# Kernel tuning notes

Measured on AMD Instinct MI355X. Metric: run time of the kernel, lower is better.

Reference implementation:

```python
import jax, jax.numpy as jnp
import numpy as np

NEIGHBOR_N = 3


def setup_inputs() -> dict:
    key = jax.random.key(0)
    ks = jax.random.split(key, 4)
    B, D = 8192, 512
    H = D // 2
    sess_emb = jax.random.normal(ks[0], (B, D), dtype=jnp.float32)
    pool_emb = jax.random.normal(ks[1], (1024, D), dtype=jnp.float32)
    # torch Linear default init ~ U(-1/sqrt(fan_in), 1/sqrt(fan_in)); scaled normals ok as baseline
    W1 = jax.random.normal(ks[2], (D, H), dtype=jnp.float32) / np.sqrt(D)
    b1 = jnp.zeros((H,), dtype=jnp.float32)
    W2 = jax.random.normal(ks[3], (H, D), dtype=jnp.float32) / np.sqrt(H)
    b2 = jnp.zeros((D,), dtype=jnp.float32)
    return {"sess_emb": sess_emb, "pool_emb": pool_emb, "W1": W1, "b1": b1, "W2": W2, "b2": b2}


def reference(sess_emb, pool_emb, W1, b1, W2, b2):
    # scoring MLP (dropout = identity in eval mode)
    h = jax.nn.relu(sess_emb @ W1 + b1)          # (B, D/2)
    sess_proj = h @ W2 + b2                       # (B, D)
    # self-similarity and top-k neighbors
    sim_matrix = sess_proj @ sess_proj.T          # (B, B)
    cos_topk, topk_indice = jax.lax.top_k(sim_matrix, NEIGHBOR_N)  # (B, K)
    sess_topk = sess_emb[topk_indice]             # (B, K, D) gather
    cos_topk = jax.nn.softmax(cos_topk, axis=-1)  # (B, K)
    neighbor_sess = jnp.einsum('bk,bkd->bd', cos_topk, sess_topk)  # (B, D)
    return (sess_topk, neighbor_sess, cos_topk)
```

## Files before the change

### kernel.cpp

```cpp
#include <hip/hip_runtime.h>
#include <hip/hip_bf16.h>
#include <math.h>

#define NB 8192
#define DD 512
#define HH 256
#define TB 128
#define BK 32
#define BK2 64
#define KT2 (DD / BK2)
#define NSLOT 64
#define ROWKEYS (NSLOT * 3)
#define NCAND 8
#define NTRI 2080

typedef unsigned short ushortT;
typedef __attribute__((ext_vector_type(8))) short bf16x8;
typedef __attribute__((ext_vector_type(4))) float f32x4;

#define AS1(p) ((const __attribute__((address_space(1))) void*)(p))
#define AS3(p) ((__attribute__((address_space(3))) void*)(p))

__device__ __forceinline__ ushortT bf16rne(float f) {
    unsigned u = __float_as_uint(f);
    unsigned r = u + 0x7FFFu + ((u >> 16) & 1u);
    return (ushortT)(r >> 16);
}
__device__ __forceinline__ float bf16tof(ushortT h) {
    return __uint_as_float(((unsigned)h) << 16);
}

__global__ __launch_bounds__(256)
void prep_kernel(const float* __restrict__ sess, const float* __restrict__ W1,
                 const float* __restrict__ W2,
                 ushortT* __restrict__ sess_hi, ushortT* __restrict__ sess_lo,
                 ushortT* __restrict__ w1t_hi, ushortT* __restrict__ w1t_lo,
                 ushortT* __restrict__ w2t_hi, ushortT* __restrict__ w2t_lo) {
    const int b = blockIdx.x, t = threadIdx.x;
    if (b < 2048) {
        size_t i = (size_t)b * 2048 + t * 8;
        float4 f0 = *(const float4*)&sess[i];
        float4 f1 = *(const float4*)&sess[i + 4];
        float f[8] = {f0.x, f0.y, f0.z, f0.w, f1.x, f1.y, f1.z, f1.w};
        unsigned hp[4], lp[4];
#pragma unroll
        for (int j = 0; j < 4; ++j) {
            ushortT h0 = bf16rne(f[2 * j]), h1 = bf16rne(f[2 * j + 1]);
            ushortT l0 = bf16rne(f[2 * j] - bf16tof(h0));
            ushortT l1 = bf16rne(f[2 * j + 1] - bf16tof(h1));
            hp[j] = (unsigned)h0 | ((unsigned)h1 << 16);
            lp[j] = (unsigned)l0 | ((unsigned)l1 << 16);
        }
        *(uint4*)&sess_hi[i] = *(uint4*)hp;
        *(uint4*)&sess_lo[i] = *(uint4*)lp;
    } else if (b < 2112) {
        int o = (b - 2048) * 2048 + t * 8;
        int k = o >> 8, c = o & 255;
        float4 f0 = *(const float4*)&W1[(size_t)k * 256 + c];
        float4 f1 = *(const float4*)&W1[(size_t)k * 256 + c + 4];
        float f[8] = {f0.x, f0.y, f0.z, f0.w, f1.x, f1.y, f1.z, f1.w};
#pragma unroll
        for (int j = 0; j < 8; ++j) {
            ushortT h = bf16rne(f[j]);
            w1t_hi[(size_t)(c + j) * 512 + k] = h;
            w1t_lo[(size_t)(c + j) * 512 + k] = bf16rne(f[j] - bf16tof(h));
        }
    } else {
        int o = (b - 2112) * 2048 + t * 8;
        int k = o >> 9, c = o & 511;
        float4 f0 = *(const float4*)&W2[(size_t)k * 512 + c];
        float4 f1 = *(const float4*)&W2[(size_t)k * 512 + c + 4];
        float f[8] = {f0.x, f0.y, f0.z, f0.w, f1.x, f1.y, f1.z, f1.w};
#pragma unroll
        for (int j = 0; j < 8; ++j) {
            ushortT h = bf16rne(f[j]);
            w2t_hi[(size_t)(c + j) * 256 + k] = h;
            w2t_lo[(size_t)(c + j) * 256 + k] = bf16rne(f[j] - bf16tof(h));
        }
    }
}

template <int KDIM, int NOUT, int EPI, int TM>
__global__ __launch_bounds__(256)
void mlp_gemm(const ushortT* __restrict__ Ahi, const ushortT* __restrict__ Alo,
              const ushortT* __restrict__ Bhi, const ushortT* __restrict__ Blo,
              const float* __restrict__ bias,
              ushortT* __restrict__ Ohi, ushortT* __restrict__ Olo,
              float* __restrict__ Of, ushortT* __restrict__ Ob) {
    constexpr int AC = TM / 16;
    constexpr int CHUNKS = 2 * AC + 32;
    constexpr int QN = CHUNKS / 4;
    constexpr int BUFS = CHUNKS * 512;
    constexpr int MI = TM / 32;
    __shared__ short gsmem[2 * BUFS];
    const int KTILES = KDIM / BK;
    const int t = threadIdx.x;
    const int w = t >> 6, l = t & 63;
    const int wr = w >> 1, wc = w & 1;
    const int tx = l & 15, tg = l >> 4;
    const int rb = blockIdx.x * TM;
    const int cb = blockIdx.y * 256;

    const int rin = l >> 2;
    const int tgs = (l & 3) ^ ((rin >> 1) & 3);
    const int loff = tx * BK + ((tg ^ ((tx >> 1) & 3)) << 3);

    f32x4 acc[MI][8];
#pragma unroll
    for (int i = 0; i < MI; ++i)
#pragma unroll
        for (int j = 0; j < 8; ++j) acc[i][j] = (f32x4){0.f, 0.f, 0.f, 0.f};

#define GSTAGE(buf, k0v)                                                                     \
    {                                                                                        \
        _Pragma("unroll")                                                                    \
        for (int q = 0; q < QN; ++q) {                                                       \
            int c = w * QN + q;                                                              \
            const ushortT* src; int row; int lofs;                                           \
            if (c < AC)            { src = Ahi; row = rb + c * 16 + rin;             lofs = c * 512; }                  \
            else if (c < 2 * AC)   { src = Alo; row = rb + (c - AC) * 16 + rin;      lofs = c * 512; }                  \
            else if (c < 2*AC+16)  { src = Bhi; row = cb + (c - 2*AC) * 16 + rin;    lofs = c * 512; }                  \
            else                   { src = Blo; row = cb + (c - 2*AC - 16) * 16 + rin; lofs = c * 512; }                \
            const ushortT* g = src + (size_t)row * KDIM + (k0v) + tgs * 8;                   \
            __builtin_amdgcn_global_load_lds(AS1(g), AS3(gsmem + (buf) * BUFS + lofs + l * 8), 16, 0, 0); \
        }                                                                                    \
    }

#define GCOMPUTE(kt)                                                                         \
    {                                                                                        \
        const short* Bu = gsmem + ((kt) & 1) * BUFS;                                         \
        bf16x8 ah[MI], al[MI], bh[8], bl[8];                                                 \
        _Pragma("unroll")                                                                    \
        for (int mi = 0; mi < MI; ++mi) {                                                    \
            ah[mi] = *(const bf16x8*)&Bu[(wr * MI + mi) * 512 + loff];                       \
            al[mi] = *(const bf16x8*)&Bu[AC * 512 + (wr * MI + mi) * 512 + loff];            \
        }                                                                                    \
        _Pragma("unroll")                                                                    \
        for (int nj = 0; nj < 8; ++nj) {                                                     \
            bh[nj] = *(const bf16x8*)&Bu[2 * AC * 512 + (wc * 8 + nj) * 512 + loff];         \
            bl[nj] = *(const bf16x8*)&Bu[(2 * AC + 16) * 512 + (wc * 8 + nj) * 512 + loff];  \
        }                                                                                    \
        asm volatile("s_waitcnt lgkmcnt(0)" ::: "memory");                                   \
        __builtin_amdgcn_sched_barrier(0);                                                   \
        __builtin_amdgcn_s_barrier();                                                        \
        __builtin_amdgcn_sched_barrier(0);                                                   \
        _Pragma("unroll")                                                                    \
        for (int mi = 0; mi < MI; ++mi)                                                      \
            _Pragma("unroll")                                                                \
            for (int nj = 0; nj < 8; ++nj) {                                                 \
                acc[mi][nj] = __builtin_amdgcn_mfma_f32_16x16x32_bf16(ah[mi], bh[nj], acc[mi][nj], 0, 0, 0); \
                acc[mi][nj] = __builtin_amdgcn_mfma_f32_16x16x32_bf16(ah[mi], bl[nj], acc[mi][nj], 0, 0, 0); \
                acc[mi][nj] = __builtin_amdgcn_mfma_f32_16x16x32_bf16(al[mi], bh[nj], acc[mi][nj], 0, 0, 0); \
            }                                                                                \
    }

    GSTAGE(0, 0);
    for (int kt = 0; kt < KTILES - 1; ++kt) {
        GSTAGE((kt + 1) & 1, (kt + 1) * BK);
        if constexpr (TM == 64) { asm volatile("s_waitcnt vmcnt(10)" ::: "memory"); }
        else                    { asm volatile("s_waitcnt vmcnt(9)" ::: "memory"); }
        __builtin_amdgcn_sched_barrier(0);
        __builtin_amdgcn_s_barrier();
        __builtin_amdgcn_sched_barrier(0);
        GCOMPUTE(kt);
    }
    asm volatile("s_waitcnt vmcnt(0)" ::: "memory");
    __builtin_amdgcn_sched_barrier(0);
    __builtin_amdgcn_s_barrier();
    __builtin_amdgcn_sched_barrier(0);
    GCOMPUTE(KTILES - 1);
#undef GSTAGE
#undef GCOMPUTE

#pragma unroll
    for (int mi = 0; mi < MI; ++mi) {
#pragma unroll
        for (int nj = 0; nj < 8; ++nj) {
            int col = cb + wc * 128 + nj * 16 + tx;
            float bv = bias[col];
#pragma unroll
            for (int rr = 0; rr < 4; ++rr) {
                int row = rb + wr * (TM / 2) + mi * 16 + tg * 4 + rr;
                float v = acc[mi][nj][rr] + bv;
                if (EPI == 0) {
                    v = fmaxf(v, 0.f);
                    ushortT h = bf16rne(v);
                    Ohi[(size_t)row * NOUT + col] = h;
                    Olo[(size_t)row * NOUT + col] = bf16rne(v - bf16tof(h));
                } else {
                    Of[(size_t)row * NOUT + col] = v;
                    Ob[(size_t)row * NOUT + col] = bf16rne(v);
                }
            }
        }
    }
}

__device__ __forceinline__ void ins3k(unsigned key, unsigned& k0, unsigned& k1, unsigned& k2) {
    bool g0 = key > k0, g1 = key > k1, g2 = key > k2;
    k2 = g1 ? k1 : (g2 ? key : k2);
    k1 = g0 ? k0 : (g1 ? key : k1);
    k0 = g0 ? key : k0;
}
__device__ __forceinline__ void merge3k(unsigned& a0, unsigned& a1, unsigned& a2,
                                        unsigned b0, unsigned b1, unsigned b2) {
    unsigned m0 = a0 > b0 ? a0 : b0;
    bool c0 = a0 > b0;
    unsigned ca1 = c0 ? a1 : b1;
    unsigned cb0 = c0 ? b0 : a0;
    unsigned ca2 = c0 ? a2 : b2;
    unsigned cb1 = c0 ? b1 : a1;
    bool c1 = ca1 > cb0;
    unsigned m1 = c1 ? ca1 : cb0;
    unsigned x = c1 ? ca2 : ca1;
    unsigned y = c1 ? cb0 : cb1;
    unsigned m2 = x > y ? x : y;
    a0 = m0; a1 = m1; a2 = m2;
}
__device__ __forceinline__ unsigned packkey(float f, unsigned idx) {
    unsigned u = __float_as_uint(f);
    unsigned tt = (unsigned)((int)u >> 31) | 0x80000000u;
    return ((u ^ tt) & 0xFFFFE000u) | (8191u - idx);
}

__global__ __launch_bounds__(256)
void sim_mfma_kernel(const short* __restrict__ projb, unsigned* __restrict__ pkeys) {
    const int b = blockIdx.x;
    const int L = (b & 7) * 260 + (b >> 3);
    int rem = L, si = 0, sj = 0;
    for (;;) {
        int n = (si == sj) ? 36 : 64;
        if (rem < n) break;
        rem -= n;
        if (si == sj) { si = 0; ++sj; } else { ++si; }
    }
    int ci, cj;
    if (si == sj) {
        cj = 0;
        while (rem >= cj + 1) { rem -= cj + 1; ++cj; }
        ci = rem;
    } else { ci = rem & 7; cj = rem >> 3; }
    const int ib = si * 8 + ci;
    const int jbk = sj * 8 + cj;
    const bool do_tr = (ib < jbk);

    __shared__ short smem[2 * TB * BK2 * 2];
    short* As = smem;
    short* Bs = smem + 2 * TB * BK2;
    unsigned* evu = (unsigned*)smem;
    unsigned* evt = (unsigned*)smem + 3200;

    const int t = threadIdx.x;
    const int w = t >> 6, l = t & 63;
    const int wr = w >> 1, wc = w & 1;
    const int tx = l & 15, tg = l >> 4;
    const int rb = ib * TB;
    const int jb = jbk * TB;

    const int sl8 = (((l & 7) ^ (l >> 3)) << 3);
    const int sw0 = (((0 + tg) ^ (tx & 7)) << 3);
    const int sw1 = (((4 + tg) ^ (tx & 7)) << 3);

    f32x4 acc[4][4];
#pragma unroll
    for (int i = 0; i < 4; ++i)
#pragma unroll
        for (int j = 0; j < 4; ++j) acc[i][j] = (f32x4){0.f, 0.f, 0.f, 0.f};

#define STAGE(buf, k0)                                                                      \
    {                                                                                       \
        _Pragma("unroll")                                                                   \
        for (int q = 0; q < 4; ++q) {                                                       \
            int c = w * 4 + q;                                                              \
            const short* ga = projb + (size_t)(rb + c * 8 + (l >> 3)) * DD + (k0) + sl8;    \
            __builtin_amdgcn_global_load_lds(AS1(ga), AS3(As + (buf) * 8192 + c * 512 + l * 8), 16, 0, 0); \
            const short* gb = projb + (size_t)(jb + c * 8 + (l >> 3)) * DD + (k0) + sl8;    \
            __builtin_amdgcn_global_load_lds(AS1(gb), AS3(Bs + (buf) * 8192 + c * 512 + l * 8), 16, 0, 0); \
        }                                                                                   \
    }

#define COMPUTE(kt)                                                                          \
    {                                                                                        \
        const short* Ab = As + ((kt) & 1) * 8192;                                            \
        const short* Bb = Bs + ((kt) & 1) * 8192;                                            \
        bf16x8 af0[4], af1[4], bf0[4], bf1[4];                                               \
        _Pragma("unroll")                                                                    \
        for (int mi = 0; mi < 4; ++mi) {                                                     \
            int row = wr * 64 + mi * 16 + tx;                                                \
            af0[mi] = *(const bf16x8*)&Ab[row * 64 + sw0];                                   \
            af1[mi] = *(const bf16x8*)&Ab[row * 64 + sw1];                                   \
        }                                                                                    \
        _Pragma("unroll")                                                                    \
        for (int nj = 0; nj < 4; ++nj) {                                                     \
            int row = wc * 64 + nj * 16 + tx;                                                \
            bf0[nj] = *(const bf16x8*)&Bb[row * 64 + sw0];                                   \
            bf1[nj] = *(const bf16x8*)&Bb[row * 64 + sw1];                                   \
        }                                                                                    \
        asm volatile("s_waitcnt lgkmcnt(0)" ::: "memory");                                   \
        __builtin_amdgcn_sched_barrier(0);                                                   \
        __builtin_amdgcn_s_barrier();                                                        \
        __builtin_amdgcn_sched_barrier(0);                                                   \
        _Pragma("unroll")                                                                    \
        for (int mi = 0; mi < 4; ++mi)                                                       \
            _Pragma("unroll")                                                                \
            for (int nj = 0; nj < 4; ++nj)                                                   \
                acc[mi][nj] = __builtin_amdgcn_mfma_f32_16x16x32_bf16(af0[mi], bf0[nj], acc[mi][nj], 0, 0, 0); \
        _Pragma("unroll")                                                                    \
        for (int mi = 0; mi < 4; ++mi)                                                       \
            _Pragma("unroll")                                                                \
            for (int nj = 0; nj < 4; ++nj)                                                   \
                acc[mi][nj] = __builtin_amdgcn_mfma_f32_16x16x32_bf16(af1[mi], bf1[nj], acc[mi][nj], 0, 0, 0); \
    }

    STAGE(0, 0);
    for (int kt = 0; kt < KT2 - 1; ++kt) {
        STAGE((kt + 1) & 1, (kt + 1) * BK2);
        asm volatile("s_waitcnt vmcnt(8)" ::: "memory");
        __builtin_amdgcn_sched_barrier(0);
        __builtin_amdgcn_s_barrier();
        __builtin_amdgcn_sched_barrier(0);
        COMPUTE(kt);
    }
    asm volatile("s_waitcnt vmcnt(0)" ::: "memory");
    __builtin_amdgcn_sched_barrier(0);
    __builtin_amdgcn_s_barrier();
    __builtin_amdgcn_sched_barrier(0);
    COMPUTE(KT2 - 1);
#undef STAGE
#undef COMPUTE

    __syncthreads();

    unsigned cinv[4];
#pragma unroll
    for (int nj = 0; nj < 4; ++nj)
        cinv[nj] = 8191u - (unsigned)(jb + wc * 64 + nj * 16 + tx);
#pragma unroll
    for (int mi = 0; mi < 4; ++mi) {
#pragma unroll
        for (int rr = 0; rr < 4; ++rr) {
            unsigned k0 = 0, k1 = 0, k2 = 0;
#pragma unroll
            for (int nj = 0; nj < 4; ++nj) {
                unsigned u = __float_as_uint(acc[mi][nj][rr]);
                unsigned tt = (unsigned)((int)u >> 31) | 0x80000000u;
                ins3k(((u ^ tt) & 0xFFFFE000u) | cinv[nj], k0, k1, k2);
            }
#pragma unroll
            for (int s = 1; s <= 2; s <<= 1) {
                unsigned b0 = (unsigned)__shfl_xor((int)k0, s, 64);
                unsigned b1 = (unsigned)__shfl_xor((int)k1, s, 64);
                unsigned b2 = (unsigned)__shfl_xor((int)k2, s, 64);
                merge3k(k0, k1, k2, b0, b1, b2);
            }
            if ((tx & 3) == 0) {
                int lrow = wr * 64 + mi * 16 + tg * 4 + rr;
                unsigned* e = &evu[lrow * 25 + (wc * 4 + (tx >> 2)) * 3];
                e[0] = k0; e[1] = k1; e[2] = k2;
            }
        }
    }

    if (do_tr) {
#pragma unroll
        for (int nj = 0; nj < 4; ++nj) {
            unsigned k0 = 0, k1 = 0, k2 = 0;
#pragma unroll
            for (int mi = 0; mi < 4; ++mi) {
#pragma unroll
                for (int rr = 0; rr < 4; ++rr) {
                    unsigned idx = (unsigned)(rb + wr * 64 + mi * 16 + tg * 4 + rr);
                    ins3k(packkey(acc[mi][nj][rr], idx), k0, k1, k2);
                }
            }
#pragma unroll
            for (int s = 16; s <= 32; s <<= 1) {
                unsigned b0 = (unsigned)__shfl_xor((int)k0, s, 64);
                unsigned b1 = (unsigned)__shfl_xor((int)k1, s, 64);
                unsigned b2 = (unsigned)__shfl_xor((int)k2, s, 64);
                merge3k(k0, k1, k2, b0, b1, b2);
            }
            if (tg == 0) {
                int col = wc * 64 + nj * 16 + tx;
                unsigned* e = &evt[col * 6 + wr * 3];
                e[0] = k0; e[1] = k1; e[2] = k2;
            }
        }
    }
    __syncthreads();

    if (t < TB) {
        unsigned k0 = 0, k1 = 0, k2 = 0;
        const unsigned* e = &evu[t * 25];
#pragma unroll
        for (int s = 0; s < 24; ++s) ins3k(e[s], k0, k1, k2);
        unsigned* pk = pkeys + (size_t)(rb + t) * ROWKEYS + jbk * 3;
        pk[0] = k0; pk[1] = k1; pk[2] = k2;
    }
    if (do_tr && t < TB) {
        unsigned k0 = 0, k1 = 0, k2 = 0;
        const unsigned* e = &evt[t * 6];
#pragma unroll
        for (int s = 0; s < 6; ++s) ins3k(e[s], k0, k1, k2);
        unsigned* pk = pkeys + (size_t)(jb + t) * ROWKEYS + ib * 3;
        pk[0] = k0; pk[1] = k1; pk[2] = k2;
    }
}

__global__ __launch_bounds__(256)
void rerank_out_kernel(const float* __restrict__ proj, const unsigned* __restrict__ pkeys,
                       const float* __restrict__ sess, float* __restrict__ out,
                       float* __restrict__ cos_out) {
    int r = blockIdx.x * 4 + (threadIdx.x >> 6);
    int t = threadIdx.x & 63;
    const unsigned* pk = pkeys + (size_t)r * ROWKEYS;
    unsigned a0 = pk[3 * t], a1 = pk[3 * t + 1], a2 = pk[3 * t + 2];
    {
        unsigned m01 = a0 > a1 ? a0 : a1, n01 = a0 > a1 ? a1 : a0;
        unsigned m2 = n01 > a2 ? n01 : a2, n2 = n01 > a2 ? a2 : n01;
        a0 = m01 > m2 ? m01 : m2;
        a1 = m01 > m2 ? m2 : m01;
        a2 = n2;
    }
    unsigned ck[NCAND];
#pragma unroll
    for (int i = 0; i < NCAND; ++i) {
        unsigned m = a0;
#pragma unroll
        for (int s = 1; s < 64; s <<= 1) {
            unsigned o = (unsigned)__shfl_xor((int)m, s, 64);
            m = m > o ? m : o;
        }
        ck[i] = m;
        if (a0 == m) { a0 = a1; a1 = a2; a2 = 0; }
    }
    int cj[NCAND];
#pragma unroll
    for (int i = 0; i < NCAND; ++i) cj[i] = 8191 - (int)(ck[i] & 0x1FFFu);

    const float* pr = proj + (size_t)r * DD;
    float myp[8];
#pragma unroll
    for (int k = 0; k < 8; ++k) myp[k] = pr[t * 8 + k];
    double part[NCAND];
#pragma unroll
    for (int i = 0; i < NCAND; ++i) {
        const float* pc = proj + (size_t)cj[i] * DD;
        double s = 0.0;
#pragma unroll
        for (int k = 0; k < 8; ++k) s += (double)myp[k] * (double)pc[t * 8 + k];
        part[i] = s;
    }
#pragma unroll
    for (int i = 0; i < NCAND; ++i) {
#pragma unroll
        for (int s = 1; s < 64; s <<= 1) part[i] += __shfl_xor(part[i], s, 64);
    }
    double bv0 = -1e300, bv1 = -1e300, bv2 = -1e300;
    int bj0 = 0x7fffffff, bj1 = 0x7fffffff, bj2 = 0x7fffffff;
#pragma unroll
    for (int i = 0; i < NCAND; ++i) {
        double v = part[i]; int j = cj[i];
        bool g2 = (v > bv2) || (v == bv2 && j < bj2);
        bool g1 = (v > bv1) || (v == bv1 && j < bj1);
        bool g0 = (v > bv0) || (v == bv0 && j < bj0);
        if (g2) {
            if (g1) {
                if (g0) { bv2 = bv1; bj2 = bj1; bv1 = bv0; bj1 = bj0; bv0 = v; bj0 = j; }
                else    { bv2 = bv1; bj2 = bj1; bv1 = v; bj1 = j; }
            } else      { bv2 = v; bj2 = j; }
        }
    }
    double e1 = exp(bv1 - bv0), e2 = exp(bv2 - bv0);
    double inv = 1.0 / (1.0 + e1 + e2);
    float w0 = (float)inv, w1 = (float)(e1 * inv), w2 = (float)(e2 * inv);
    if (t == 0) {
        cos_out[r * 3 + 0] = w0; cos_out[r * 3 + 1] = w1; cos_out[r * 3 + 2] = w2;
    }
    const float4* s0 = (const float4*)(sess + (size_t)bj0 * DD);
    const float4* s1 = (const float4*)(sess + (size_t)bj1 * DD);
    const float4* s2 = (const float4*)(sess + (size_t)bj2 * DD);
    float4* o = (float4*)(out + (size_t)r * 3 * DD);
    float4* nb = (float4*)(out + (size_t)NB * 3 * DD + (size_t)r * DD);
#pragma unroll
    for (int e = 0; e < 2; ++e) {
        int q = t + e * 64;
        float4 x0 = s0[q], x1 = s1[q], x2 = s2[q];
        o[q] = x0; o[128 + q] = x1; o[256 + q] = x2;
        float4 v;
        v.x = fmaf(w0, x0.x, fmaf(w1, x1.x, w2 * x2.x));
        v.y = fmaf(w0, x0.y, fmaf(w1, x1.y, w2 * x2.y));
        v.z = fmaf(w0, x0.z, fmaf(w1, x1.z, w2 * x2.z));
        v.w = fmaf(w0, x0.w, fmaf(w1, x1.w, w2 * x2.w));
        nb[q] = v;
    }
}

extern "C" void kernel_launch(void* const* d_in, const int* in_sizes, int n_in,
                              void* d_out, int out_size, void* d_ws, size_t ws_size,
                              hipStream_t stream) {
    const float* sess = (const float*)d_in[0];
    const float* W1 = (const float*)d_in[2];
    const float* b1 = (const float*)d_in[3];
    const float* W2 = (const float*)d_in[4];
    const float* b2 = (const float*)d_in[5];
    float* out = (float*)d_out;

    const size_t MBc = 1u << 20;
    char* W = (char*)d_ws;
    float*   proj    = (float*)W;
    ushortT* sess_hi = (ushortT*)W;
    ushortT* sess_lo = sess_hi + (size_t)NB * DD;
    ushortT* projb   = (ushortT*)(W + 16 * MBc);
    ushortT* h_hi    = (ushortT*)(W + 24 * MBc);
    ushortT* h_lo    = (ushortT*)(W + 28 * MBc);
    ushortT* w1t_hi  = (ushortT*)(W + 32 * MBc);
    ushortT* w1t_lo  = w1t_hi + 256 * 512;
    ushortT* w2t_hi  = w1t_lo + 256 * 512;
    ushortT* w2t_lo  = w2t_hi + 512 * 256;
    unsigned* pkeys  = (unsigned*)(W + 24 * MBc);

    float* cos_out = out + (size_t)NB * 3 * DD + (size_t)NB * DD;

    hipLaunchKernelGGL(prep_kernel, dim3(2176), dim3(256), 0, stream,
                       sess, W1, W2, sess_hi, sess_lo, w1t_hi, w1t_lo, w2t_hi, w2t_lo);
    hipLaunchKernelGGL((mlp_gemm<512, 256, 0, 32>), dim3(NB / 32, 1), dim3(256), 0, stream,
                       sess_hi, sess_lo, w1t_hi, w1t_lo, b1, h_hi, h_lo, (float*)nullptr, (ushortT*)nullptr);
    hipLaunchKernelGGL((mlp_gemm<256, 512, 1, 64>), dim3(NB / 64, 2), dim3(256), 0, stream,
                       h_hi, h_lo, w2t_hi, w2t_lo, b2, (ushortT*)nullptr, (ushortT*)nullptr, proj, projb);
    hipLaunchKernelGGL(sim_mfma_kernel, dim3(NTRI), dim3(256), 0, stream,
                       (const short*)projb, pkeys);
    hipLaunchKernelGGL(rerank_out_kernel, dim3(NB / 4), dim3(256), 0, stream,
                       proj, pkeys, sess, out, cos_out);
}
```

Baseline: 145.3 us.

## Make sim kernel persistent over four tiles with cross-tile prefetch

The similarity kernel now launches 520 blocks, each handling four consecutive upper-triangle tiles. The first k-slab of the next tile is prefetched during the last compute step of the current one, hiding load latency at tile boundaries. Epilogue buffers move to dedicated LDS so they no longer alias the staging buffers, and top-3 selection uses a sorting network plus merges instead of sequential inserts. This adds LDS use, which may lower occupancy, and an extra barrier per k-step.

Result: slower. 179.3 us (+23.4%).

```diff
diff --git a/kernel.cpp b/kernel.cpp
--- a/kernel.cpp
+++ b/kernel.cpp
@@ -12,7 +12,7 @@
 #define NSLOT 64
 #define ROWKEYS (NSLOT * 3)
 #define NCAND 8
-#define NTRI 2080
+#define NBLK 520
 
 typedef unsigned short ushortT;
 typedef __attribute__((ext_vector_type(8))) short bf16x8;
@@ -196,6 +196,8 @@
     }
 }
 
+__device__ __forceinline__ unsigned umaxu(unsigned a, unsigned b) { return a > b ? a : b; }
+__device__ __forceinline__ unsigned uminu(unsigned a, unsigned b) { return a < b ? a : b; }
 __device__ __forceinline__ void ins3k(unsigned key, unsigned& k0, unsigned& k1, unsigned& k2) {
     bool g0 = key > k0, g1 = key > k1, g2 = key > k2;
     k2 = g1 ? k1 : (g2 ? key : k2);
@@ -217,16 +219,25 @@
     unsigned m2 = x > y ? x : y;
     a0 = m0; a1 = m1; a2 = m2;
 }
+__device__ __forceinline__ void top3of4(unsigned a, unsigned b, unsigned c, unsigned d,
+                                        unsigned& k0, unsigned& k1, unsigned& k2) {
+    unsigned s1 = umaxu(a, b), t1 = uminu(a, b);
+    unsigned s2 = umaxu(c, d), t2 = uminu(c, d);
+    bool cw = s1 > s2;
+    unsigned c2 = cw ? s2 : s1;
+    unsigned tw = cw ? t1 : t2;
+    unsigned tl = cw ? t2 : t1;
+    k0 = cw ? s1 : s2;
+    k1 = umaxu(c2, tw);
+    k2 = umaxu(uminu(c2, tw), tl);
+}
 __device__ __forceinline__ unsigned packkey(float f, unsigned idx) {
     unsigned u = __float_as_uint(f);
     unsigned tt = (unsigned)((int)u >> 31) | 0x80000000u;
     return ((u ^ tt) & 0xFFFFE000u) | (8191u - idx);
 }
 
-__global__ __launch_bounds__(256)
-void sim_mfma_kernel(const short* __restrict__ projb, unsigned* __restrict__ pkeys) {
-    const int b = blockIdx.x;
-    const int L = (b & 7) * 260 + (b >> 3);
+__device__ __forceinline__ void decodeL(int L, int& ib, int& jbk) {
     int rem = L, si = 0, sj = 0;
     for (;;) {
         int n = (si == sj) ? 36 : 64;
@@ -240,171 +251,183 @@
         while (rem >= cj + 1) { rem -= cj + 1; ++cj; }
         ci = rem;
     } else { ci = rem & 7; cj = rem >> 3; }
-    const int ib = si * 8 + ci;
-    const int jbk = sj * 8 + cj;
-    const bool do_tr = (ib < jbk);
-
+    ib = si * 8 + ci;
+    jbk = sj * 8 + cj;
+}
+
+__global__ __launch_bounds__(256)
+void sim_mfma_kernel(const short* __restrict__ projb, unsigned* __restrict__ pkeys) {
     __shared__ short smem[2 * TB * BK2 * 2];
+    __shared__ unsigned evu[TB * 25];
+    __shared__ unsigned evt[TB * 6];
     short* As = smem;
     short* Bs = smem + 2 * TB * BK2;
-    unsigned* evu = (unsigned*)smem;
-    unsigned* evt = (unsigned*)smem + 3200;
+
+    const int b = blockIdx.x;
+    const int base = ((b & 7) * 65 + (b >> 3)) * 4;
 
     const int t = threadIdx.x;
     const int w = t >> 6, l = t & 63;
     const int wr = w >> 1, wc = w & 1;
     const int tx = l & 15, tg = l >> 4;
-    const int rb = ib * TB;
-    const int jb = jbk * TB;
 
     const int sl8 = (((l & 7) ^ (l >> 3)) << 3);
     const int sw0 = (((0 + tg) ^ (tx & 7)) << 3);
     const int sw1 = (((4 + tg) ^ (tx & 7)) << 3);
 
-    f32x4 acc[4][4];
-#pragma unroll
-    for (int i = 0; i < 4; ++i)
-#pragma unroll
-        for (int j = 0; j < 4; ++j) acc[i][j] = (f32x4){0.f, 0.f, 0.f, 0.f};
-
-#define STAGE(buf, k0)                                                                      \
+#define STAGE(buf, k0, RB, JB)                                                              \
     {                                                                                       \
         _Pragma("unroll")                                                                   \
-        for (int q = 0; q < 4; ++q) {                                                       \
-            int c = w * 4 + q;                                                              \
-            const short* ga = projb + (size_t)(rb + c * 8 + (l >> 3)) * DD + (k0) + sl8;    \
+        for (int qq = 0; qq < 4; ++qq) {                                                    \
+            int c = w * 4 + qq;                                                             \
+            const short* ga = projb + (size_t)((RB) + c * 8 + (l >> 3)) * DD + (k0) + sl8;  \
             __builtin_amdgcn_global_load_lds(AS1(ga), AS3(As + (buf) * 8192 + c * 512 + l * 8), 16, 0, 0); \
-            const short* gb = projb + (size_t)(jb + c * 8 + (l >> 3)) * DD + (k0) + sl8;    \
+            const short* gb = projb + (size_t)((JB) + c * 8 + (l >> 3)) * DD + (k0) + sl8;  \
             __builtin_amdgcn_global_load_lds(AS1(gb), AS3(Bs + (buf) * 8192 + c * 512 + l * 8), 16, 0, 0); \
         }                                                                                   \
     }
 
-#define COMPUTE(kt)                                                                          \
-    {                                                                                        \
-        const short* Ab = As + ((kt) & 1) * 8192;                                            \
-        const short* Bb = Bs + ((kt) & 1) * 8192;                                            \
-        bf16x8 af0[4], af1[4], bf0[4], bf1[4];                                               \
-        _Pragma("unroll")                                                                    \
-        for (int mi = 0; mi < 4; ++mi) {                                                     \
-            int row = wr * 64 + mi * 16 + tx;                                                \
-            af0[mi] = *(const bf16x8*)&Ab[row * 64 + sw0];                                   \
-            af1[mi] = *(const bf16x8*)&Ab[row * 64 + sw1];                                   \
-        }                                                                                    \
-        _Pragma("unroll")                                                                    \
-        for (int nj = 0; nj < 4; ++nj) {                                                     \
-            int row = wc * 64 + nj * 16 + tx;                                                \
-            bf0[nj] = *(const bf16x8*)&Bb[row * 64 + sw0];                                   \
-            bf1[nj] = *(const bf16x8*)&Bb[row * 64 + sw1];                                   \
-        }                                                                                    \
-        asm volatile("s_waitcnt lgkmcnt(0)" ::: "memory");                                   \
-        __builtin_amdgcn_sched_barrier(0);                                                   \
-        __builtin_amdgcn_s_barrier();                                                        \
-        __builtin_amdgcn_sched_barrier(0);                                                   \
-        _Pragma("unroll")                                                                    \
-        for (int mi = 0; mi < 4; ++mi)                                                       \
-            _Pragma("unroll")                                                                \
-            for (int nj = 0; nj < 4; ++nj)                                                   \
-                acc[mi][nj] = __builtin_amdgcn_mfma_f32_16x16x32_bf16(af0[mi], bf0[nj], acc[mi][nj], 0, 0, 0); \
-        _Pragma("unroll")                                                                    \
-        for (int mi = 0; mi < 4; ++mi)                                                       \
-            _Pragma("unroll")                                                                \
-            for (int nj = 0; nj < 4; ++nj)                                                   \
-                acc[mi][nj] = __builtin_amdgcn_mfma_f32_16x16x32_bf16(af1[mi], bf1[nj], acc[mi][nj], 0, 0, 0); \
-    }
-
-    STAGE(0, 0);
-    for (int kt = 0; kt < KT2 - 1; ++kt) {
-        STAGE((kt + 1) & 1, (kt + 1) * BK2);
-        asm volatile("s_waitcnt vmcnt(8)" ::: "memory");
-        __builtin_amdgcn_sched_barrier(0);
-        __builtin_amdgcn_s_barrier();
-        __builtin_amdgcn_sched_barrier(0);
-        COMPUTE(kt);
-    }
-    asm volatile("s_waitcnt vmcnt(0)" ::: "memory");
-    __builtin_amdgcn_sched_barrier(0);
-    __builtin_amdgcn_s_barrier();
-    __builtin_amdgcn_sched_barrier(0);
-    COMPUTE(KT2 - 1);
+    int ib, jbk;
+    decodeL(base, ib, jbk);
+    int rb = ib * TB, jb = jbk * TB;
+    STAGE(0, 0, rb, jb);
+
+    for (int q = 0; q < 4; ++q) {
+        const bool do_tr = (ib < jbk);
+        int nib = 0, njbk = 0;
+        if (q < 3) decodeL(base + q + 1, nib, njbk);
+
+        f32x4 acc[4][4];
+#pragma unroll
+        for (int i = 0; i < 4; ++i)
+#pragma unroll
+            for (int j = 0; j < 4; ++j) acc[i][j] = (f32x4){0.f, 0.f, 0.f, 0.f};
+
+        for (int kt = 0; kt < KT2; ++kt) {
+            if (kt + 1 < KT2) { STAGE((kt + 1) & 1, (kt + 1) * BK2, rb, jb); }
+            else if (q < 3)   { STAGE(0, 0, nib * TB, njbk * TB); }
+            if (kt + 1 < KT2 || q < 3) { asm volatile("s_waitcnt vmcnt(8)" ::: "memory"); }
+            else                       { asm volatile("s_waitcnt vmcnt(0)" ::: "memory"); }
+            __builtin_amdgcn_sched_barrier(0);
+            __builtin_amdgcn_s_barrier();
+            __builtin_amdgcn_sched_barrier(0);
+            {
+                const short* Ab = As + (kt & 1) * 8192;
+                const short* Bb = Bs + (kt & 1) * 8192;
+                bf16x8 af0[4], af1[4], bf0[4], bf1[4];
+#pragma unroll
+                for (int mi = 0; mi < 4; ++mi) {
+                    int row = wr * 64 + mi * 16 + tx;
+                    af0[mi] = *(const bf16x8*)&Ab[row * 64 + sw0];
+                    af1[mi] = *(const bf16x8*)&Ab[row * 64 + sw1];
+                }
+#pragma unroll
+                for (int nj = 0; nj < 4; ++nj) {
+                    int row = wc * 64 + nj * 16 + tx;
+                    bf0[nj] = *(const bf16x8*)&Bb[row * 64 + sw0];
+                    bf1[nj] = *(const bf16x8*)&Bb[row * 64 + sw1];
+                }
+#pragma unroll
+                for (int mi = 0; mi < 4; ++mi)
+#pragma unroll
+                    for (int nj = 0; nj < 4; ++nj)
+                        acc[mi][nj] = __builtin_amdgcn_mfma_f32_16x16x32_bf16(af0[mi], bf0[nj], acc[mi][nj], 0, 0, 0);
+#pragma unroll
+                for (int mi = 0; mi < 4; ++mi)
+#pragma unroll
+                    for (int nj = 0; nj < 4; ++nj)
+                        acc[mi][nj] = __builtin_amdgcn_mfma_f32_16x16x32_bf16(af1[mi], bf1[nj], acc[mi][nj], 0, 0, 0);
+            }
+            __builtin_amdgcn_sched_barrier(0);
+            __builtin_amdgcn_s_barrier();
+            __builtin_amdgcn_sched_barrier(0);
+        }
+
+        unsigned cinv[4];
+#pragma unroll
+        for (int nj = 0; nj < 4; ++nj)
+            cinv[nj] = 8191u - (unsigned)(jb + wc * 64 + nj * 16 + tx);
+#pragma unroll
+        for (int mi = 0; mi < 4; ++mi) {
+#pragma unroll
+            for (int rr = 0; rr < 4; ++rr) {
+                unsigned kk[4];
+#pragma unroll
+                for (int nj = 0; nj < 4; ++nj) {
+                    unsigned u = __float_as_uint(acc[mi][nj][rr]);
+                    unsigned tt = (unsigned)((int)u >> 31) | 0x80000000u;
+                    kk[nj] = ((u ^ tt) & 0xFFFFE000u) | cinv[nj];
+                }
+                unsigned k0, k1, k2;
+                top3of4(kk[0], kk[1], kk[2], kk[3], k0, k1, k2);
+#pragma unroll
+                for (int s = 1; s <= 2; s <<= 1) {
+                    unsigned b0 = (unsigned)__shfl_xor((int)k0, s, 64);
+                    unsigned b1 = (unsigned)__shfl_xor((int)k1, s, 64);
+                    unsigned b2 = (unsigned)__shfl_xor((int)k2, s, 64);
+                    merge3k(k0, k1, k2, b0, b1, b2);
+                }
+                if ((tx & 3) == 0) {
+                    int lrow = wr * 64 + mi * 16 + tg * 4 + rr;
+                    unsigned* e = &evu[lrow * 25 + (wc * 4 + (tx >> 2)) * 3];
+                    e[0] = k0; e[1] = k1; e[2] = k2;
+                }
+            }
+        }
+
+        if (do_tr) {
+#pragma unroll
+            for (int nj = 0; nj < 4; ++nj) {
+                unsigned v[16];
+#pragma unroll
+                for (int mi = 0; mi < 4; ++mi)
+#pragma unroll
+                    for (int rr = 0; rr < 4; ++rr) {
+                        unsigned idx = (unsigned)(rb + wr * 64 + mi * 16 + tg * 4 + rr);
+                        v[mi * 4 + rr] = packkey(acc[mi][nj][rr], idx);
+                    }
+                unsigned x0, x1, x2, y0, y1, y2, z0, z1, z2;
+                top3of4(v[0], v[1], v[2], v[3], x0, x1, x2);
+                top3of4(v[4], v[5], v[6], v[7], y0, y1, y2);
+                merge3k(x0, x1, x2, y0, y1, y2);
+                top3of4(v[8], v[9], v[10], v[11], y0, y1, y2);
+                top3of4(v[12], v[13], v[14], v[15], z0, z1, z2);
+                merge3k(y0, y1, y2, z0, z1, z2);
+                merge3k(x0, x1, x2, y0, y1, y2);
+#pragma unroll
+                for (int s = 16; s <= 32; s <<= 1) {
+                    unsigned b0 = (unsigned)__shfl_xor((int)x0, s, 64);
+                    unsigned b1 = (unsigned)__shfl_xor((int)x1, s, 64);
+                    unsigned b2 = (unsigned)__shfl_xor((int)x2, s, 64);
+                    merge3k(x0, x1, x2, b0, b1, b2);
+                }
+                if (tg == 0) {
+                    int col = wc * 64 + nj * 16 + tx;
+                    unsigned* e = &evt[col * 6 + wr * 3];
+                    e[0] = x0; e[1] = x1; e[2] = x2;
+                }
+            }
+        }
+        __syncthreads();
+
+        if (t < TB) {
+            const unsigned* e = &evu[t * 25];
+            unsigned k0 = e[0], k1 = e[1], k2 = e[2];
+#pragma unroll
+            for (int s = 1; s < 8; ++s) merge3k(k0, k1, k2, e[s * 3], e[s * 3 + 1], e[s * 3 + 2]);
+            unsigned* pk = pkeys + (size_t)(rb + t) * ROWKEYS + jbk * 3;
+            pk[0] = k0; pk[1] = k1; pk[2] = k2;
+        }
+        if (do_tr && t < TB) {
+            const unsigned* e = &evt[t * 6];
+            unsigned k0 = e[0], k1 = e[1], k2 = e[2];
+            merge3k(k0, k1, k2, e[3], e[4], e[5]);
+            unsigned* pk = pkeys + (size_t)(jb + t) * ROWKEYS + ib * 3;
+            pk[0] = k0; pk[1] = k1; pk[2] = k2;
+        }
+        ib = nib; jbk = njbk; rb = ib * TB; jb = jbk * TB;
+    }
 #undef STAGE
-#undef COMPUTE
-
-    __syncthreads();
-
-    unsigned cinv[4];
-#pragma unroll
-    for (int nj = 0; nj < 4; ++nj)
-        cinv[nj] = 8191u - (unsigned)(jb + wc * 64 + nj * 16 + tx);
-#pragma unroll
-    for (int mi = 0; mi < 4; ++mi) {
-#pragma unroll
-        for (int rr = 0; rr < 4; ++rr) {
-            unsigned k0 = 0, k1 = 0, k2 = 0;
-#pragma unroll
-            for (int nj = 0; nj < 4; ++nj) {
-                unsigned u = __float_as_uint(acc[mi][nj][rr]);
-                unsigned tt = (unsigned)((int)u >> 31) | 0x80000000u;
-                ins3k(((u ^ tt) & 0xFFFFE000u) | cinv[nj], k0, k1, k2);
-            }
-#pragma unroll
-            for (int s = 1; s <= 2; s <<= 1) {
-                unsigned b0 = (unsigned)__shfl_xor((int)k0, s, 64);
-                unsigned b1 = (unsigned)__shfl_xor((int)k1, s, 64);
-                unsigned b2 = (unsigned)__shfl_xor((int)k2, s, 64);
-                merge3k(k0, k1, k2, b0, b1, b2);
-            }
-            if ((tx & 3) == 0) {
-                int lrow = wr * 64 + mi * 16 + tg * 4 + rr;
-                unsigned* e = &evu[lrow * 25 + (wc * 4 + (tx >> 2)) * 3];
-                e[0] = k0; e[1] = k1; e[2] = k2;
-            }
-        }
-    }
-
-    if (do_tr) {
-#pragma unroll
-        for (int nj = 0; nj < 4; ++nj) {
-            unsigned k0 = 0, k1 = 0, k2 = 0;
-#pragma unroll
-            for (int mi = 0; mi < 4; ++mi) {
-#pragma unroll
-                for (int rr = 0; rr < 4; ++rr) {
-                    unsigned idx = (unsigned)(rb + wr * 64 + mi * 16 + tg * 4 + rr);
-                    ins3k(packkey(acc[mi][nj][rr], idx), k0, k1, k2);
-                }
-            }
-#pragma unroll
-            for (int s = 16; s <= 32; s <<= 1) {
-                unsigned b0 = (unsigned)__shfl_xor((int)k0, s, 64);
-                unsigned b1 = (unsigned)__shfl_xor((int)k1, s, 64);
-                unsigned b2 = (unsigned)__shfl_xor((int)k2, s, 64);
-                merge3k(k0, k1, k2, b0, b1, b2);
-            }
-            if (tg == 0) {
-                int col = wc * 64 + nj * 16 + tx;
-                unsigned* e = &evt[col * 6 + wr * 3];
-                e[0] = k0; e[1] = k1; e[2] = k2;
-            }
-        }
-    }
-    __syncthreads();
-
-    if (t < TB) {
-        unsigned k0 = 0, k1 = 0, k2 = 0;
-        const unsigned* e = &evu[t * 25];
-#pragma unroll
-        for (int s = 0; s < 24; ++s) ins3k(e[s], k0, k1, k2);
-        unsigned* pk = pkeys + (size_t)(rb + t) * ROWKEYS + jbk * 3;
-        pk[0] = k0; pk[1] = k1; pk[2] = k2;
-    }
-    if (do_tr && t < TB) {
-        unsigned k0 = 0, k1 = 0, k2 = 0;
-        const unsigned* e = &evt[t * 6];
-#pragma unroll
-        for (int s = 0; s < 6; ++s) ins3k(e[s], k0, k1, k2);
-        unsigned* pk = pkeys + (size_t)(jb + t) * ROWKEYS + ib * 3;
-        pk[0] = k0; pk[1] = k1; pk[2] = k2;
-    }
 }
 
 __global__ __launch_bounds__(256)
@@ -528,7 +551,7 @@
                        sess_hi, sess_lo, w1t_hi, w1t_lo, b1, h_hi, h_lo, (float*)nullptr, (ushortT*)nullptr);
     hipLaunchKernelGGL((mlp_gemm<256, 512, 1, 64>), dim3(NB / 64, 2), dim3(256), 0, stream,
                        h_hi, h_lo, w2t_hi, w2t_lo, b2, (ushortT*)nullptr, (ushortT*)nullptr, proj, projb);
-    hipLaunchKernelGGL(sim_mfma_kernel, dim3(NTRI), dim3(256), 0, stream,
+    hipLaunchKernelGGL(sim_mfma_kernel, dim3(NBLK), dim3(256), 0, stream,
                        (const short*)projb, pkeys);
     hipLaunchKernelGGL(rerank_out_kernel, dim3(NB / 4), dim3(256), 0, stream,
                        proj, pkeys, sess, out, cos_out);
```
